# Optimization experiments

Measured on AMD Instinct MI355X. Metric: run time of the kernel, lower is better.

## Reference

```python
import jax, jax.numpy as jnp
import numpy as np

N_NODES, N_EDGES, F_IN, HID, PROJ, N_CLS, N_GRAPHS, T_EMB = 50000, 800000, 128, 128, 512, 32, 256, 768
EPS_BN, EPS_LN = 1e-5, 1e-5


def setup_inputs() -> dict:
    key = jax.random.key(0)
    ks = jax.random.split(key, 24)
    s = 0.05
    inp = {
        "x": jax.random.normal(ks[0], (N_NODES, F_IN), jnp.float32),
        "edge_index": jax.random.randint(ks[1], (2, N_EDGES), 0, N_NODES),
        "batch": jnp.sort(jax.random.randint(ks[2], (N_NODES,), 0, N_GRAPHS)),
        "text_feats": jax.random.normal(ks[3], (N_GRAPHS, T_EMB), jnp.float32),
        # 4 stacked GCN layers (all 128->128), each with BatchNorm affine params
        "gcn_W": jax.random.normal(ks[4], (4, F_IN, HID), jnp.float32) * s,
        "gcn_b": jnp.zeros((4, HID), jnp.float32),
        "bn_g": jnp.ones((4, HID), jnp.float32),
        "bn_b": jnp.zeros((4, HID), jnp.float32),
        # graph projection head
        "gpj_W1": jax.random.normal(ks[5], (HID, PROJ), jnp.float32) * s,
        "gpj_b1": jnp.zeros((PROJ,), jnp.float32),
        "gpj_W2": jax.random.normal(ks[6], (PROJ, PROJ), jnp.float32) * s,
        "gpj_b2": jnp.zeros((PROJ,), jnp.float32),
        "gpj_g": jnp.ones((PROJ,), jnp.float32),
        "gpj_be": jnp.zeros((PROJ,), jnp.float32),
        "gcl_W": jax.random.normal(ks[7], (PROJ, N_CLS), jnp.float32) * s,
        "gcl_b": jnp.zeros((N_CLS,), jnp.float32),
        # text projection head
        "tpj_W1": jax.random.normal(ks[8], (T_EMB, PROJ), jnp.float32) * s,
        "tpj_b1": jnp.zeros((PROJ,), jnp.float32),
        "tpj_W2": jax.random.normal(ks[9], (PROJ, PROJ), jnp.float32) * s,
        "tpj_b2": jnp.zeros((PROJ,), jnp.float32),
        "tpj_g": jnp.ones((PROJ,), jnp.float32),
        "tpj_be": jnp.zeros((PROJ,), jnp.float32),
        "tcl_W": jax.random.normal(ks[10], (PROJ, N_CLS), jnp.float32) * s,
        "tcl_b": jnp.zeros((N_CLS,), jnp.float32),
    }
    return inp


def _gcn_layer(x, src, dst, dnorm, W, b):
    # PyG GCNConv with self-loops and symmetric normalization
    xw = x @ W  # [N, H]
    coef = dnorm[src] * dnorm[dst]  # [E]
    agg = jax.ops.segment_sum(xw[src] * coef[:, None], dst, num_segments=N_NODES)
    agg = agg + xw * (dnorm * dnorm)[:, None]  # self-loop contribution
    return agg + b


def _batch_norm(x, g, b):
    mu = jnp.mean(x, axis=0)
    var = jnp.mean((x - mu) ** 2, axis=0)
    return (x - mu) * jax.lax.rsqrt(var + EPS_BN) * g + b


def _projection_head(x, W1, b1, W2, b2, g, be):
    projected = x @ W1 + b1
    h = jax.nn.gelu(projected, approximate=False)
    h = h @ W2 + b2
    h = h + projected  # residual (dropout in eval mode = identity)
    mu = jnp.mean(h, axis=-1, keepdims=True)
    var = jnp.mean((h - mu) ** 2, axis=-1, keepdims=True)
    return (h - mu) * jax.lax.rsqrt(var + EPS_LN) * g + be


def reference(x, edge_index, batch, text_feats, gcn_W, gcn_b, bn_g, bn_b,
              gpj_W1, gpj_b1, gpj_W2, gpj_b2, gpj_g, gpj_be, gcl_W, gcl_b,
              tpj_W1, tpj_b1, tpj_W2, tpj_b2, tpj_g, tpj_be, tcl_W, tcl_b):
    src, dst = edge_index[0], edge_index[1]
    deg = jax.ops.segment_sum(jnp.ones((N_EDGES,), x.dtype), dst, num_segments=N_NODES) + 1.0
    dnorm = jax.lax.rsqrt(deg)
    h = x
    for i in range(4):  # input block, 2 hidden blocks, output block
        h = _gcn_layer(h, src, dst, dnorm, gcn_W[i], gcn_b[i])
        h = jax.nn.leaky_relu(h, negative_slope=0.01)
        h = _batch_norm(h, bn_g[i], bn_b[i])
    # global mean pool over graphs
    sums = jax.ops.segment_sum(h, batch, num_segments=N_GRAPHS)
    cnts = jax.ops.segment_sum(jnp.ones((N_NODES,), h.dtype), batch, num_segments=N_GRAPHS)
    g_emb = sums / jnp.maximum(cnts, 1.0)[:, None]  # [G, HID]

    graph_proj = _projection_head(g_emb, gpj_W1, gpj_b1, gpj_W2, gpj_b2, gpj_g, gpj_be)
    graph_logp = jax.nn.log_softmax(graph_proj @ gcl_W + gcl_b, axis=-1)

    text_proj = _projection_head(text_feats, tpj_W1, tpj_b1, tpj_W2, tpj_b2, tpj_g, tpj_be)
    text_logp = jax.nn.log_softmax(text_proj @ tcl_W + tcl_b, axis=-1)

    return (graph_proj, text_proj, graph_logp, text_logp)
```

## Files before the change

### kernel.cpp

```cpp
#include <hip/hip_runtime.h>
#include <hip/hip_bf16.h>

#define N_NODES 50000
#define N_EDGES 800000
#define F_IN    128
#define HID     128
#define PROJ    512
#define N_CLS   32
#define N_GRAPHS 256
#define T_EMB   768
#define NB_SCAN ((N_NODES + 255) / 256)
#define DBINS   1024
#define NBROW   ((N_NODES + 63) / 64)
#define NBG2    ((NBROW + 1) / 2)

typedef __attribute__((ext_vector_type(8))) short bf16x8;
typedef __attribute__((ext_vector_type(4))) float f32x4;

__device__ __forceinline__ float bf2f(unsigned short u) {
    unsigned v = ((unsigned)u) << 16;
    return __uint_as_float(v);
}
__device__ __forceinline__ unsigned short f2us(float v) {
    __hip_bfloat16 b = __float2bfloat16(v);
    union { __hip_bfloat16 b; unsigned short u; } c; c.b = b; return c.u;
}

__global__ void k_deg(const int* __restrict__ ei, int* __restrict__ cnt, int nE) {
    int e = blockIdx.x * 256 + threadIdx.x;
    if (e < nE) atomicAdd(cnt + ei[nE + e], 1);
}

__global__ __launch_bounds__(256) void k_scan1(const int* __restrict__ cnt,
    int* __restrict__ rowstart, float* __restrict__ dnorm, int* __restrict__ bsum)
{
    __shared__ int ps[256];
    int t = threadIdx.x;
    int i = blockIdx.x * 256 + t;
    int c = (i < N_NODES) ? cnt[i] : 0;
    if (i < N_NODES) dnorm[i] = rsqrtf((float)c + 1.0f);
    ps[t] = c;
    __syncthreads();
    for (int off = 1; off < 256; off <<= 1) {
        int v = (t >= off) ? ps[t - off] : 0;
        __syncthreads();
        ps[t] += v;
        __syncthreads();
    }
    if (i < N_NODES) rowstart[i] = ps[t] - c;
    if (t == 255) bsum[blockIdx.x] = ps[255];
}

__global__ __launch_bounds__(256) void k_scan2(int* __restrict__ bsum) {
    __shared__ int ps[256];
    int t = threadIdx.x;
    int v = (t < NB_SCAN) ? bsum[t] : 0;
    ps[t] = v;
    __syncthreads();
    for (int off = 1; off < 256; off <<= 1) {
        int u = (t >= off) ? ps[t - off] : 0;
        __syncthreads();
        ps[t] += u;
        __syncthreads();
    }
    if (t < NB_SCAN) bsum[t] = ps[t] - v;
}

__global__ __launch_bounds__(256) void k_scan3(int* __restrict__ rowstart,
    const int* __restrict__ bsum, const int* __restrict__ cnt,
    int* __restrict__ dhist)
{
    __shared__ int lh[DBINS];
    int t = threadIdx.x;
    for (int k = t; k < DBINS; k += 256) lh[k] = 0;
    __syncthreads();
    int i = blockIdx.x * 256 + t;
    if (i < N_NODES) {
        rowstart[i] += bsum[blockIdx.x];
        atomicAdd(&lh[min(cnt[i], DBINS - 1)], 1);
    }
    if (i == 0) rowstart[N_NODES] = N_EDGES;
    __syncthreads();
    for (int k = t; k < DBINS; k += 256) {
        int v = lh[k];
        if (v) atomicAdd(dhist + k, v);
    }
}

__global__ __launch_bounds__(256) void k_dscan(const int* __restrict__ dhist,
                                               int* __restrict__ doff) {
    __shared__ int part[256];
    __shared__ int binv[DBINS];
    int t = threadIdx.x;
    int base = t * 4;
    int g0 = dhist[DBINS - 1 - (base + 0)];
    int g1 = dhist[DBINS - 1 - (base + 1)];
    int g2 = dhist[DBINS - 1 - (base + 2)];
    int g3 = dhist[DBINS - 1 - (base + 3)];
    int s = g0 + g1 + g2 + g3;
    part[t] = s;
    __syncthreads();
    for (int off = 1; off < 256; off <<= 1) {
        int v = (t >= off) ? part[t - off] : 0;
        __syncthreads();
        part[t] += v;
        __syncthreads();
    }
    int run = part[t] - s;
    binv[base + 0] = run; run += g0;
    binv[base + 1] = run; run += g1;
    binv[base + 2] = run; run += g2;
    binv[base + 3] = run; run += g3;
    __syncthreads();
    for (int k = t; k < DBINS; k += 256) doff[DBINS - 1 - k] = binv[k];
}

__global__ __launch_bounds__(1024) void k_dperm(const int* __restrict__ cnt,
    int* __restrict__ doff, int* __restrict__ rowperm)
{
    __shared__ int lh[DBINS];
    __shared__ int lbase[DBINS];
    int t = threadIdx.x;
    if (t < DBINS) lh[t] = 0;
    __syncthreads();
    int i = blockIdx.x * 1024 + t;
    int bin = 0, lrank = 0;
    bool ok = i < N_NODES;
    if (ok) {
        bin = min(cnt[i], DBINS - 1);
        lrank = atomicAdd(&lh[bin], 1);
    }
    __syncthreads();
    if (t < DBINS) {
        int v = lh[t];
        if (v) lbase[t] = atomicAdd(doff + t, v);
    }
    __syncthreads();
    if (ok) rowperm[lbase[bin] + lrank] = i;
}

__global__ void k_fill(const int* __restrict__ ei, const int* __restrict__ rowstart,
                       int* __restrict__ cursor, int* __restrict__ srcl, int nE) {
    int e = blockIdx.x * 256 + threadIdx.x;
    if (e >= nE) return;
    int s = ei[e];
    int d = ei[nE + e];
    int pos = rowstart[d] + atomicAdd(cursor + d, 1);
    srcl[pos] = s;
}

__global__ void k_prep(const float* __restrict__ W, unsigned short* __restrict__ Wt,
                       const int* __restrict__ batch, int* __restrict__ gstart) {
    int t = blockIdx.x * 256 + threadIdx.x;
    if (t < 4 * 128 * 128) {
        int l = t >> 14;
        int k = (t >> 7) & 127;
        int n = t & 127;
        Wt[(size_t)l * 16384 + n * 128 + k] = f2us(W[(size_t)l * 16384 + k * 128 + n]);
    } else {
        int r = t - 4 * 128 * 128;
        if (r <= N_NODES) {
            int b  = (r < N_NODES) ? batch[r] : N_GRAPHS;
            int bp = (r > 0) ? batch[r - 1] : -1;
            for (int g = bp + 1; g <= b && g <= N_GRAPHS; g++) gstart[g] = r;
        }
    }
}

__global__ __launch_bounds__(256) void k_gcn_mm_mfma(const void* __restrict__ inp,
    const unsigned short* __restrict__ Wt,
    const float* __restrict__ stats, const float* __restrict__ bng,
    const float* __restrict__ bnb, const float* __restrict__ dnorm,
    unsigned short* __restrict__ ph, int n)
{
    __shared__ __align__(16) unsigned short Bs[128][136];
    __shared__ float scs[128], shs[128];
    int t = threadIdx.x;
    int row0 = blockIdx.x * 64;

    if (stats && t < 128) {
        float inv_n = 1.0f / (float)N_NODES;
        float mu = stats[t] * inv_n;
        float var = stats[128 + t] * inv_n - mu * mu;
        float rs = rsqrtf(var + 1e-5f);
        float sc = rs * bng[t];
        scs[t] = sc;
        shs[t] = bnb[t] - mu * sc;
    }
#pragma unroll
    for (int i = 0; i < 8; i++) {
        int c = t + i * 256;
        int nn = c >> 4;
        int k8 = (c & 15) * 8;
        *(uint4*)&Bs[nn][k8] = *(const uint4*)(Wt + (size_t)nn * 128 + k8);
    }
    __syncthreads();

    int w = t >> 6, lane = t & 63;
    int m = lane & 15, quad = lane >> 4;
    int arow = row0 + w * 16 + m;
    bool rowok = arow < n;

    bf16x8 afrag[4];
    if (!stats) {
        const float* inf = (const float*)inp;
#pragma unroll
        for (int ki = 0; ki < 4; ki++) {
            int k8 = ki * 32 + quad * 8;
            float4 v0 = make_float4(0.f, 0.f, 0.f, 0.f);
            float4 v1 = make_float4(0.f, 0.f, 0.f, 0.f);
            if (rowok) {
                v0 = *(const float4*)(inf + (size_t)arow * 128 + k8);
                v1 = *(const float4*)(inf + (size_t)arow * 128 + k8 + 4);
            }
            union { unsigned short u[8]; bf16x8 v; } pk;
            pk.u[0] = f2us(v0.x); pk.u[1] = f2us(v0.y); pk.u[2] = f2us(v0.z); pk.u[3] = f2us(v0.w);
            pk.u[4] = f2us(v1.x); pk.u[5] = f2us(v1.y); pk.u[6] = f2us(v1.z); pk.u[7] = f2us(v1.w);
            afrag[ki] = pk.v;
        }
    } else {
        const unsigned short* inb = (const unsigned short*)inp;
#pragma unroll
        for (int ki = 0; ki < 4; ki++) {
            int k8 = ki * 32 + quad * 8;
            uint4 raw = make_uint4(0, 0, 0, 0);
            if (rowok) raw = *(const uint4*)(inb + (size_t)arow * 128 + k8);
            unsigned rr[4] = { raw.x, raw.y, raw.z, raw.w };
            union { unsigned short u[8]; bf16x8 v; } pk;
#pragma unroll
            for (int j = 0; j < 4; j++) {
                int f0 = k8 + 2 * j, f1 = k8 + 2 * j + 1;
                float a0 = bf2f((unsigned short)rr[j]) * scs[f0] + shs[f0];
                float a1 = bf2f((unsigned short)(rr[j] >> 16)) * scs[f1] + shs[f1];
                pk.u[2 * j] = f2us(a0);
                pk.u[2 * j + 1] = f2us(a1);
            }
            afrag[ki] = pk.v;
        }
    }

    f32x4 acc[8];
#pragma unroll
    for (int nt = 0; nt < 8; nt++) acc[nt] = (f32x4){0.f, 0.f, 0.f, 0.f};
#pragma unroll
    for (int ki = 0; ki < 4; ki++) {
#pragma unroll
        for (int nt = 0; nt < 8; nt++) {
            bf16x8 b = *(const bf16x8*)&Bs[nt * 16 + m][ki * 32 + quad * 8];
            acc[nt] = __builtin_amdgcn_mfma_f32_16x16x32_bf16(afrag[ki], b, acc[nt], 0, 0, 0);
        }
    }

    float dn[4];
#pragma unroll
    for (int reg = 0; reg < 4; reg++) {
        int gr = row0 + w * 16 + quad * 4 + reg;
        dn[reg] = (gr < n) ? dnorm[gr] : 0.f;
    }

    __syncthreads();
#pragma unroll
    for (int nt = 0; nt < 8; nt++) {
#pragma unroll
        for (int reg = 0; reg < 4; reg++) {
            Bs[w * 16 + quad * 4 + reg][nt * 16 + m] = f2us(acc[nt][reg] * dn[reg]);
        }
    }
    __syncthreads();
#pragma unroll
    for (int i = 0; i < 4; i++) {
        int idx = t + i * 256;
        int r = idx >> 4;
        int c8 = (idx & 15) * 8;
        int gr = row0 + r;
        int ch = c8 >> 5;
        int off = c8 & 31;
        if (gr < n)
            *(uint4*)(ph + (size_t)ch * (N_NODES * 32) + (size_t)gr * 32 + off)
                = *(const uint4*)&Bs[r][c8];
    }
}

__global__ __launch_bounds__(256) void k_gather_c(const uint4* __restrict__ ph128,
    const int* __restrict__ srcl, const int* __restrict__ rowstart,
    const int* __restrict__ rowperm, const float* __restrict__ dnorm,
    const float* __restrict__ bias, unsigned short* __restrict__ outbb,
    float* __restrict__ stats, int n)
{
    const int EMAX = N_EDGES - 1;
    __shared__ float bsm[32], bqm[32];
    int t = threadIdx.x;
    if (t < 32) { bsm[t] = 0.f; bqm[t] = 0.f; }
    __syncthreads();

    int bx = blockIdx.x;
    int xcd = bx & 7;
    int c = xcd >> 1;
    int rb = (bx >> 3) * 2 + (xcd & 1);
    if (rb >= NBROW) return;
    int lane = t & 63;
    int w = t >> 6;
    int grp = lane >> 2;
    int l4 = lane & 3;
    int idx = rb * 64 + w * 16 + grp;
    bool rok = idx < n;
    int r = rok ? rowperm[idx] : 0;
    int start = rowstart[r];
    int deg = rowstart[r + 1] - start;
    float dnr = dnorm[r];
    if (!rok) { deg = 0; dnr = 0.f; }
    int len = deg + 1;

    const uint4* phc = ph128 + (size_t)c * (N_NODES * 4);

    float bi[8];
#pragma unroll
    for (int k = 0; k < 8; k++) bi[k] = bias[c * 32 + l4 * 8 + k];

    float a[8];
#pragma unroll
    for (int k = 0; k < 8; k++) a[k] = 0.f;

    for (int j = 0; j < len; j += 4) {
        uint4 uv[4];
#pragma unroll
        for (int u = 0; u < 4; u++) {
            int i = j + u;
            int sl = srcl[min(start + i, EMAX)];
            int s = (i < deg) ? sl : r;
            uv[u] = phc[(size_t)s * 4 + l4];
        }
#pragma unroll
        for (int u = 0; u < 4; u++) {
            int i = j + u;
            float wt = (i < len) ? 1.f : 0.f;
            unsigned rr[4] = { uv[u].x, uv[u].y, uv[u].z, uv[u].w };
#pragma unroll
            for (int d = 0; d < 4; d++) {
                a[2 * d]     += wt * bf2f((unsigned short)rr[d]);
                a[2 * d + 1] += wt * bf2f((unsigned short)(rr[d] >> 16));
            }
        }
    }

    float v[8];
#pragma unroll
    for (int k = 0; k < 8; k++) {
        float x = a[k] * dnr + bi[k];
        v[k] = x > 0.f ? x : 0.01f * x;
    }
    if (rok) {
        union { unsigned short us[8]; uint4 u; } ov;
#pragma unroll
        for (int k = 0; k < 8; k++) ov.us[k] = f2us(v[k]);
        *(uint4*)(outbb + (size_t)r * 128 + c * 32 + l4 * 8) = ov.u;
    } else {
#pragma unroll
        for (int k = 0; k < 8; k++) v[k] = 0.f;
    }

    float q[8];
#pragma unroll
    for (int k = 0; k < 8; k++) q[k] = v[k] * v[k];
#pragma unroll
    for (int mk = 4; mk < 64; mk <<= 1) {
#pragma unroll
        for (int k = 0; k < 8; k++) {
            v[k] += __shfl_xor(v[k], mk, 64);
            q[k] += __shfl_xor(q[k], mk, 64);
        }
    }
    if (grp == 0) {
#pragma unroll
        for (int k = 0; k < 8; k++) {
            atomicAdd(&bsm[l4 * 8 + k], v[k]);
            atomicAdd(&bqm[l4 * 8 + k], q[k]);
        }
    }
    __syncthreads();
    if (t < 32) {
        atomicAdd(&stats[c * 32 + t], bsm[t]);
        atomicAdd(&stats[128 + c * 32 + t], bqm[t]);
    }
}

__global__ __launch_bounds__(256) void k_pool2(const unsigned short* __restrict__ outbb,
    const int* __restrict__ gstart, const float* __restrict__ stats,
    const float* __restrict__ bng, const float* __restrict__ bnb,
    float* __restrict__ gemb)
{
    __shared__ float scs[128], shs[128];
    int g = blockIdx.x;
    int t = threadIdx.x;
    if (t < 128) {
        float inv_n = 1.0f / (float)N_NODES;
        float mu = stats[t] * inv_n;
        float var = stats[128 + t] * inv_n - mu * mu;
        float rs = rsqrtf(var + 1e-5f);
        float sc = rs * bng[t];
        scs[t] = sc;
        shs[t] = bnb[t] - mu * sc;
    }
    __syncthreads();
    int f = t & 127;
    int half = t >> 7;
    int start = gstart[g], end = gstart[g + 1];
    int cnt = end - start;
    float s0 = 0.f, s1 = 0.f, s2 = 0.f, s3 = 0.f;
    int r = start + half;
    for (; r + 6 < end; r += 8) {
        s0 += bf2f(outbb[(size_t)(r    ) * 128 + f]);
        s1 += bf2f(outbb[(size_t)(r + 2) * 128 + f]);
        s2 += bf2f(outbb[(size_t)(r + 4) * 128 + f]);
        s3 += bf2f(outbb[(size_t)(r + 6) * 128 + f]);
    }
    for (; r < end; r += 2) s0 += bf2f(outbb[(size_t)r * 128 + f]);
    float sum = (s0 + s1) + (s2 + s3);
    __shared__ float sb[256];
    sb[t] = sum;
    __syncthreads();
    if (t < 128) {
        float tot = sb[t] + sb[t + 128];
        float v = (cnt > 0) ? (tot / (float)cnt) * scs[f] + shs[f] : 0.f;
        gemb[(size_t)g * 128 + f] = v;
    }
}

__global__ __launch_bounds__(256) void k_head1x(const float* __restrict__ gemb,
    const float* __restrict__ textf,
    const float* __restrict__ gW1, const float* __restrict__ gb1,
    const float* __restrict__ tW1, const float* __restrict__ tb1,
    float* __restrict__ projg, float* __restrict__ projt)
{
    __shared__ float ins[8][768];
    int bx = blockIdx.x;
    int chunk = blockIdx.y;
    int isT = bx >= 32;
    int rb = isT ? bx - 32 : bx;
    const float* in = isT ? textf : gemb;
    int K = isT ? T_EMB : HID;
    const float* W = isT ? tW1 : gW1;
    const float* b = isT ? tb1 : gb1;
    float* outp = isT ? projt : projg;

    int t = threadIdx.x;
    int tot = 8 * K;
    for (int l = t; l < tot; l += 256) {
        int r = l / K, k = l - r * K;
        ins[r][k] = in[(size_t)(rb * 8 + r) * K + k];
    }
    __syncthreads();
    int col = chunk * 128 + (t & 127);
    int rg = t >> 7;
    float acc[4] = { 0.f, 0.f, 0.f, 0.f };
    for (int k = 0; k < K; k++) {
        float w = W[(size_t)k * 512 + col];
#pragma unroll
        for (int i = 0; i < 4; i++) acc[i] += ins[rg * 4 + i][k] * w;
    }
    float bias = b[col];
#pragma unroll
    for (int i = 0; i < 4; i++) {
        int row = rb * 8 + rg * 4 + i;
        outp[(size_t)row * 512 + col] = acc[i] + bias;
    }
}

__global__ __launch_bounds__(256) void k_head2c(
    const float* __restrict__ projg, const float* __restrict__ projt,
    const float* __restrict__ gW2, const float* __restrict__ gb2,
    const float* __restrict__ gg, const float* __restrict__ gbe,
    const float* __restrict__ gclW, const float* __restrict__ gclb,
    const float* __restrict__ tW2, const float* __restrict__ tb2,
    const float* __restrict__ tg, const float* __restrict__ tbe,
    const float* __restrict__ tclW, const float* __restrict__ tclb,
    float* __restrict__ o_gproj, float* __restrict__ o_tproj,
    float* __restrict__ o_glogp, float* __restrict__ o_tlogp)
{
    __shared__ float prow[512], grow[512], onorm[512], red[256];
    __shared__ float part[8][32];
    __shared__ float logits[32];
    __shared__ float mred, lred;
    int bx = blockIdx.x;
    int isT = bx >= N_GRAPHS;
    int row = isT ? bx - N_GRAPHS : bx;
    const float* proj = isT ? projt : projg;
    const float* W2 = isT ? tW2 : gW2;
    const float* b2 = isT ? tb2 : gb2;
    const float* g  = isT ? tg  : gg;
    const float* be = isT ? tbe : gbe;
    const float* Wc = isT ? tclW : gclW;
    const float* bc = isT ? tclb : gclb;
    float* oproj = isT ? o_tproj : o_gproj;
    float* ologp = isT ? o_tlogp : o_glogp;

    int t = threadIdx.x;
    for (int c = t; c < 512; c += 256) {
        float p = proj[(size_t)row * 512 + c];
        prow[c] = p;
        grow[c] = 0.5f * p * (1.0f + erff(p * 0.70710678118f));
    }
    __syncthreads();
    float a0 = 0.f, a1 = 0.f;
    int c0 = t, c1 = t + 256;
    for (int k = 0; k < 512; k++) {
        float gk = grow[k];
        a0 += gk * W2[(size_t)k * 512 + c0];
        a1 += gk * W2[(size_t)k * 512 + c1];
    }
    float h0 = a0 + b2[c0] + prow[c0];
    float h1 = a1 + b2[c1] + prow[c1];
    red[t] = h0 + h1;
    __syncthreads();
    for (int s = 128; s > 0; s >>= 1) { if (t < s) red[t] += red[t + s]; __syncthreads(); }
    float mu = red[0] * (1.0f / 512.0f);
    __syncthreads();
    float d0 = h0 - mu, d1 = h1 - mu;
    red[t] = d0 * d0 + d1 * d1;
    __syncthreads();
    for (int s = 128; s > 0; s >>= 1) { if (t < s) red[t] += red[t + s]; __syncthreads(); }
    float rs = rsqrtf(red[0] * (1.0f / 512.0f) + 1e-5f);
    float o0 = d0 * rs * g[c0] + be[c0];
    float o1 = d1 * rs * g[c1] + be[c1];
    onorm[c0] = o0;
    onorm[c1] = o1;
    oproj[(size_t)row * 512 + c0] = o0;
    oproj[(size_t)row * 512 + c1] = o1;
    __syncthreads();

    int c = t & 31, seg = t >> 5;
    float p = 0.f;
    for (int k = seg * 64; k < seg * 64 + 64; k++)
        p += onorm[k] * Wc[(size_t)k * 32 + c];
    part[seg][c] = p;
    __syncthreads();
    if (t < 32) {
        float l = bc[t];
#pragma unroll
        for (int s = 0; s < 8; s++) l += part[s][t];
        logits[t] = l;
    }
    __syncthreads();
    if (t == 0) {
        float m = logits[0];
        for (int i = 1; i < 32; i++) m = fmaxf(m, logits[i]);
        float sum = 0.f;
        for (int i = 0; i < 32; i++) sum += expf(logits[i] - m);
        mred = m; lred = logf(sum);
    }
    __syncthreads();
    if (t < 32) ologp[(size_t)row * 32 + t] = logits[t] - mred - lred;
}

extern "C" void kernel_launch(void* const* d_in, const int* in_sizes, int n_in,
                              void* d_out, int out_size, void* d_ws, size_t ws_size,
                              hipStream_t stream) {
    const float* x     = (const float*)d_in[0];
    const int*   ei    = (const int*)d_in[1];
    const int*   batch = (const int*)d_in[2];
    const float* textf = (const float*)d_in[3];
    const float* gcnW  = (const float*)d_in[4];
    const float* gcnb  = (const float*)d_in[5];
    const float* bng   = (const float*)d_in[6];
    const float* bnb   = (const float*)d_in[7];
    const float* gW1   = (const float*)d_in[8];
    const float* gb1   = (const float*)d_in[9];
    const float* gW2   = (const float*)d_in[10];
    const float* gb2   = (const float*)d_in[11];
    const float* gg    = (const float*)d_in[12];
    const float* gbe   = (const float*)d_in[13];
    const float* gclW  = (const float*)d_in[14];
    const float* gclb  = (const float*)d_in[15];
    const float* tW1   = (const float*)d_in[16];
    const float* tb1   = (const float*)d_in[17];
    const float* tW2   = (const float*)d_in[18];
    const float* tb2   = (const float*)d_in[19];
    const float* tg    = (const float*)d_in[20];
    const float* tbe   = (const float*)d_in[21];
    const float* tclW  = (const float*)d_in[22];
    const float* tclb  = (const float*)d_in[23];

    const int N = N_NODES, E = N_EDGES;
    const int NF = N * HID;

    float* p = (float*)d_ws;
    unsigned short* outbb = (unsigned short*)p; p += NF / 2;
    unsigned short* ph    = (unsigned short*)p; p += NF / 2;
    unsigned short* Wt    = (unsigned short*)p; p += 4 * 16384 / 2;
    float* dnorm = p; p += N;
    float* gemb  = p; p += N_GRAPHS * HID;
    float* projg = p; p += N_GRAPHS * PROJ;
    float* projt = p; p += N_GRAPHS * PROJ;
    int* cnt      = (int*)p; p += N;
    int* cursor   = (int*)p; p += N;
    float* stats4 = p; p += 4 * 256;
    int* dhist    = (int*)p; p += DBINS;
    int* rowstart = (int*)p; p += N + 1;
    int* gstart   = (int*)p; p += N_GRAPHS + 1;
    int* bsum     = (int*)p; p += 256;
    int* srcl     = (int*)p; p += E;
    int* doff     = (int*)p; p += DBINS;
    int* rowperm  = (int*)p; p += N;

    float* outp = (float*)d_out;
    float* o_gproj = outp;
    float* o_tproj = outp + N_GRAPHS * PROJ;
    float* o_glogp = o_tproj + N_GRAPHS * PROJ;
    float* o_tlogp = o_glogp + N_GRAPHS * N_CLS;

    hipMemsetAsync(cnt, 0, (size_t)(2 * N + 4 * 256 + DBINS) * sizeof(int), stream);
    k_deg<<<(E + 255) / 256, 256, 0, stream>>>(ei, cnt, E);
    k_scan1<<<NB_SCAN, 256, 0, stream>>>(cnt, rowstart, dnorm, bsum);
    k_scan2<<<1, 256, 0, stream>>>(bsum);
    k_scan3<<<NB_SCAN, 256, 0, stream>>>(rowstart, bsum, cnt, dhist);
    k_fill<<<(E + 255) / 256, 256, 0, stream>>>(ei, rowstart, cursor, srcl, E);
    k_dscan<<<1, 256, 0, stream>>>(dhist, doff);
    k_dperm<<<(N + 1023) / 1024, 1024, 0, stream>>>(cnt, doff, rowperm);
    k_prep<<<(4 * 16384 + N + 1 + 255) / 256, 256, 0, stream>>>(gcnW, Wt, batch, gstart);

    for (int l = 0; l < 4; l++) {
        const void* in = (l == 0) ? (const void*)x : (const void*)outbb;
        const float* st = (l == 0) ? nullptr : stats4 + (l - 1) * 256;
        const float* bg = (l == 0) ? nullptr : bng + (size_t)(l - 1) * HID;
        const float* bb = (l == 0) ? nullptr : bnb + (size_t)(l - 1) * HID;
        k_gcn_mm_mfma<<<(N + 63) / 64, 256, 0, stream>>>(in, Wt + (size_t)l * 16384,
                                                         st, bg, bb, dnorm, ph, N);
        k_gather_c<<<NBG2 * 8, 256, 0, stream>>>((const uint4*)ph, srcl,
                                                 rowstart, rowperm, dnorm,
                                                 gcnb + (size_t)l * HID, outbb,
                                                 stats4 + l * 256, N);
    }

    k_pool2<<<N_GRAPHS, 256, 0, stream>>>(outbb, gstart, stats4 + 3 * 256,
                                          bng + 3 * HID, bnb + 3 * HID, gemb);

    k_head1x<<<dim3(64, 4), 256, 0, stream>>>(gemb, textf, gW1, gb1, tW1, tb1, projg, projt);
    k_head2c<<<2 * N_GRAPHS, 256, 0, stream>>>(projg, projt,
                                               gW2, gb2, gg, gbe, gclW, gclb,
                                               tW2, tb2, tg, tbe, tclW, tclb,
                                               o_gproj, o_tproj, o_glogp, o_tlogp);
}
```

Measured before the change: 490.8 us.

## Partition degree/fill atomics by destination range and split head1 K dimension

The degree-count and CSR-fill kernels now launch eight blocks per 4096-edge slice. Each block handles only destinations in one eighth of the node range, so a block's atomics land in a smaller region of memory, which should improve L2 locality. The cost is that every edge index is read eight times. The text projection's first GEMM is split into six K-chunks across a third grid dimension, which adds parallelism; the partial sums and bias are then added inside head2. This uses extra workspace and adds reads of the six partial buffers.

```diff
diff --git a/kernel.cpp b/kernel.cpp
--- a/kernel.cpp
+++ b/kernel.cpp
@@ -13,6 +13,8 @@
 #define DBINS   1024
 #define NBROW   ((N_NODES + 63) / 64)
 #define NBG2    ((NBROW + 1) / 2)
+#define SHW     6250
+#define ESLICE  ((N_EDGES + 4095) / 4096)
 
 typedef __attribute__((ext_vector_type(8))) short bf16x8;
 typedef __attribute__((ext_vector_type(4))) float f32x4;
@@ -26,9 +28,21 @@
     union { __hip_bfloat16 b; unsigned short u; } c; c.b = b; return c.u;
 }
 
-__global__ void k_deg(const int* __restrict__ ei, int* __restrict__ cnt, int nE) {
-    int e = blockIdx.x * 256 + threadIdx.x;
-    if (e < nE) atomicAdd(cnt + ei[nE + e], 1);
+__global__ __launch_bounds__(256) void k_deg(const int* __restrict__ ei,
+                                             int* __restrict__ cnt, int nE) {
+    int bx = blockIdx.x;
+    int s = bx & 7;
+    int slice = bx >> 3;
+    int lo = s * SHW, hi = lo + SHW;
+    int base = slice * 4096 + threadIdx.x;
+#pragma unroll 4
+    for (int u = 0; u < 16; u++) {
+        int e = base + u * 256;
+        if (e < nE) {
+            int d = ei[nE + e];
+            if (d >= lo && d < hi) atomicAdd(cnt + d, 1);
+        }
+    }
 }
 
 __global__ __launch_bounds__(256) void k_scan1(const int* __restrict__ cnt,
@@ -139,14 +153,26 @@
     if (ok) rowperm[lbase[bin] + lrank] = i;
 }
 
-__global__ void k_fill(const int* __restrict__ ei, const int* __restrict__ rowstart,
-                       int* __restrict__ cursor, int* __restrict__ srcl, int nE) {
-    int e = blockIdx.x * 256 + threadIdx.x;
-    if (e >= nE) return;
-    int s = ei[e];
-    int d = ei[nE + e];
-    int pos = rowstart[d] + atomicAdd(cursor + d, 1);
-    srcl[pos] = s;
+__global__ __launch_bounds__(256) void k_fill(const int* __restrict__ ei,
+    const int* __restrict__ rowstart, int* __restrict__ cursor,
+    int* __restrict__ srcl, int nE)
+{
+    int bx = blockIdx.x;
+    int s = bx & 7;
+    int slice = bx >> 3;
+    int lo = s * SHW, hi = lo + SHW;
+    int base = slice * 4096 + threadIdx.x;
+#pragma unroll 4
+    for (int u = 0; u < 16; u++) {
+        int e = base + u * 256;
+        if (e < nE) {
+            int d = ei[nE + e];
+            if (d >= lo && d < hi) {
+                int pos = rowstart[d] + atomicAdd(cursor + d, 1);
+                srcl[pos] = ei[e];
+            }
+        }
+    }
 }
 
 __global__ void k_prep(const float* __restrict__ W, unsigned short* __restrict__ Wt,
@@ -428,46 +454,47 @@
 
 __global__ __launch_bounds__(256) void k_head1x(const float* __restrict__ gemb,
     const float* __restrict__ textf,
-    const float* __restrict__ gW1, const float* __restrict__ gb1,
-    const float* __restrict__ tW1, const float* __restrict__ tb1,
-    float* __restrict__ projg, float* __restrict__ projt)
-{
-    __shared__ float ins[8][768];
+    const float* __restrict__ gW1, const float* __restrict__ tW1,
+    float* __restrict__ projg, float* __restrict__ projt6)
+{
+    __shared__ float ins[8][128];
     int bx = blockIdx.x;
-    int chunk = blockIdx.y;
+    int kc = blockIdx.z;
     int isT = bx >= 32;
+    if (!isT && kc > 0) return;
     int rb = isT ? bx - 32 : bx;
     const float* in = isT ? textf : gemb;
     int K = isT ? T_EMB : HID;
     const float* W = isT ? tW1 : gW1;
-    const float* b = isT ? tb1 : gb1;
-    float* outp = isT ? projt : projg;
-
-    int t = threadIdx.x;
-    int tot = 8 * K;
-    for (int l = t; l < tot; l += 256) {
-        int r = l / K, k = l - r * K;
-        ins[r][k] = in[(size_t)(rb * 8 + r) * K + k];
-    }
-    __syncthreads();
-    int col = chunk * 128 + (t & 127);
+    float* outp = isT ? (projt6 + (size_t)kc * (N_GRAPHS * PROJ)) : projg;
+    int k0 = kc * 128;
+
+    int t = threadIdx.x;
+    {
+        int r = t >> 5, k = (t & 31) * 4;
+        *(float4*)&ins[r][k] = *(const float4*)(in + (size_t)(rb * 8 + r) * K + k0 + k);
+    }
+    __syncthreads();
+    int col = blockIdx.y * 128 + (t & 127);
     int rg = t >> 7;
     float acc[4] = { 0.f, 0.f, 0.f, 0.f };
-    for (int k = 0; k < K; k++) {
-        float w = W[(size_t)k * 512 + col];
+    const float* Wp = W + (size_t)k0 * 512 + col;
+#pragma unroll 8
+    for (int k = 0; k < 128; k++) {
+        float w = Wp[(size_t)k * 512];
 #pragma unroll
         for (int i = 0; i < 4; i++) acc[i] += ins[rg * 4 + i][k] * w;
     }
-    float bias = b[col];
 #pragma unroll
     for (int i = 0; i < 4; i++) {
         int row = rb * 8 + rg * 4 + i;
-        outp[(size_t)row * 512 + col] = acc[i] + bias;
+        outp[(size_t)row * 512 + col] = acc[i];
     }
 }
 
 __global__ __launch_bounds__(256) void k_head2c(
-    const float* __restrict__ projg, const float* __restrict__ projt,
+    const float* __restrict__ projg, const float* __restrict__ projt6,
+    const float* __restrict__ gb1, const float* __restrict__ tb1,
     const float* __restrict__ gW2, const float* __restrict__ gb2,
     const float* __restrict__ gg, const float* __restrict__ gbe,
     const float* __restrict__ gclW, const float* __restrict__ gclb,
@@ -484,7 +511,7 @@
     int bx = blockIdx.x;
     int isT = bx >= N_GRAPHS;
     int row = isT ? bx - N_GRAPHS : bx;
-    const float* proj = isT ? projt : projg;
+    const float* b1 = isT ? tb1 : gb1;
     const float* W2 = isT ? tW2 : gW2;
     const float* b2 = isT ? tb2 : gb2;
     const float* g  = isT ? tg  : gg;
@@ -496,7 +523,16 @@
 
     int t = threadIdx.x;
     for (int c = t; c < 512; c += 256) {
-        float p = proj[(size_t)row * 512 + c];
+        float p;
+        if (isT) {
+            const float* pp = projt6 + (size_t)row * 512 + c;
+            p = pp[0];
+#pragma unroll
+            for (int s = 1; s < 6; s++) p += pp[(size_t)s * (N_GRAPHS * PROJ)];
+        } else {
+            p = projg[(size_t)row * 512 + c];
+        }
+        p += b1[c];
         prow[c] = p;
         grow[c] = 0.5f * p * (1.0f + erff(p * 0.70710678118f));
     }
@@ -587,10 +623,10 @@
     unsigned short* outbb = (unsigned short*)p; p += NF / 2;
     unsigned short* ph    = (unsigned short*)p; p += NF / 2;
     unsigned short* Wt    = (unsigned short*)p; p += 4 * 16384 / 2;
-    float* dnorm = p; p += N;
-    float* gemb  = p; p += N_GRAPHS * HID;
-    float* projg = p; p += N_GRAPHS * PROJ;
-    float* projt = p; p += N_GRAPHS * PROJ;
+    float* dnorm  = p; p += N;
+    float* gemb   = p; p += N_GRAPHS * HID;
+    float* projg  = p; p += N_GRAPHS * PROJ;
+    float* projt6 = p; p += 6 * N_GRAPHS * PROJ;
     int* cnt      = (int*)p; p += N;
     int* cursor   = (int*)p; p += N;
     float* stats4 = p; p += 4 * 256;
@@ -609,11 +645,11 @@
     float* o_tlogp = o_glogp + N_GRAPHS * N_CLS;
 
     hipMemsetAsync(cnt, 0, (size_t)(2 * N + 4 * 256 + DBINS) * sizeof(int), stream);
-    k_deg<<<(E + 255) / 256, 256, 0, stream>>>(ei, cnt, E);
+    k_deg<<<ESLICE * 8, 256, 0, stream>>>(ei, cnt, E);
     k_scan1<<<NB_SCAN, 256, 0, stream>>>(cnt, rowstart, dnorm, bsum);
     k_scan2<<<1, 256, 0, stream>>>(bsum);
     k_scan3<<<NB_SCAN, 256, 0, stream>>>(rowstart, bsum, cnt, dhist);
-    k_fill<<<(E + 255) / 256, 256, 0, stream>>>(ei, rowstart, cursor, srcl, E);
+    k_fill<<<ESLICE * 8, 256, 0, stream>>>(ei, rowstart, cursor, srcl, E);
     k_dscan<<<1, 256, 0, stream>>>(dhist, doff);
     k_dperm<<<(N + 1023) / 1024, 1024, 0, stream>>>(cnt, doff, rowperm);
     k_prep<<<(4 * 16384 + N + 1 + 255) / 256, 256, 0, stream>>>(gcnW, Wt, batch, gstart);
@@ -634,8 +670,8 @@
     k_pool2<<<N_GRAPHS, 256, 0, stream>>>(outbb, gstart, stats4 + 3 * 256,
                                           bng + 3 * HID, bnb + 3 * HID, gemb);
 
-    k_head1x<<<dim3(64, 4), 256, 0, stream>>>(gemb, textf, gW1, gb1, tW1, tb1, projg, projt);
-    k_head2c<<<2 * N_GRAPHS, 256, 0, stream>>>(projg, projt,
+    k_head1x<<<dim3(64, 4, 6), 256, 0, stream>>>(gemb, textf, gW1, tW1, projg, projt6);
+    k_head2c<<<2 * N_GRAPHS, 256, 0, stream>>>(projg, projt6, gb1, tb1,
                                                gW2, gb2, gg, gbe, gclW, gclb,
                                                tW2, tb2, tg, tbe, tclW, tclb,
                                                o_gproj, o_tproj, o_glogp, o_tlogp);
```

Result: faster. 462.9 us (-5.7%).
